# Kernel optimization log

Hardware: AMD Instinct MI355X
Metric: run time of the kernel (lower is better)

## Reference

```python
import jax, jax.numpy as jnp
import numpy as np

B, H, S, D = 4, 16, 2048, 64
INV_SCALE_FACTOR = 8.0  # scores are divided by this (== sqrt(D))
DROPOUT_P = 0.0         # deterministic baseline; dropout is identity at p=0


def setup_inputs() -> dict:
    key = jax.random.key(0)
    kq, kk, kv = jax.random.split(key, 3)
    return {
        "query": jax.random.normal(kq, (B, H, S, D), dtype=jnp.float32),
        "key": jax.random.normal(kk, (B, H, S, D), dtype=jnp.float32),
        "value": jax.random.normal(kv, (B, H, S, D), dtype=jnp.float32),
    }


def reference(query, key, value):
    # scores: [B, H, Sq, Sk]
    scores = jnp.einsum("bhqd,bhkd->bhqk", query, key) / INV_SCALE_FACTOR
    probs = jax.nn.softmax(scores, axis=-1)
    # dropout_p == 0.0 -> identity
    out = jnp.einsum("bhqk,bhkd->bhqd", probs, value)
    return out
```

## Files before the change

### kernel.cpp

```cpp
#include <hip/hip_runtime.h>


#define S_LEN 2048
#define D_DIM 64
#define TK    64
#define NTILE (S_LEN / TK)
#define LOG2E_OVER8 0.18033688011112042f
#define VROW  72
#define VTILE (64 * VROW)
#define VBH   (NTILE * VTILE)

typedef __bf16 bf16x8 __attribute__((ext_vector_type(8)));
typedef __bf16 bf16x4 __attribute__((ext_vector_type(4)));
typedef short  s16x4  __attribute__((ext_vector_type(4)));
typedef float  f32x4  __attribute__((ext_vector_type(4)));
typedef unsigned short us;

__device__ __forceinline__ us f2bf(float f) {
    union { __bf16 h; us u; } c;
    c.h = (__bf16)f;
    return c.u;
}

__device__ __forceinline__ unsigned pk2(float a, float b) {
#if __has_builtin(__builtin_amdgcn_cvt_pk_bf16_f32)
    typedef __bf16 bf2 __attribute__((ext_vector_type(2)));
    union { bf2 h; unsigned u; } c;
    c.h = __builtin_amdgcn_cvt_pk_bf16_f32(a, b);
    return c.u;
#else
    return ((unsigned)f2bf(b) << 16) | f2bf(a);
#endif
}

__device__ __forceinline__ float fast_exp2(float x) {
#if __has_builtin(__builtin_amdgcn_exp2f)
    return __builtin_amdgcn_exp2f(x);
#else
    return exp2f(x);
#endif
}

__device__ __forceinline__ void gload_lds16(const void* g, void* l) {
    __builtin_amdgcn_global_load_lds(
        (const __attribute__((address_space(1))) unsigned int*)g,
        (__attribute__((address_space(3))) unsigned int*)l, 16, 0, 0);
}

__device__ __forceinline__ f32x4 mfma16x16x16(s16x4 a, s16x4 b, f32x4 c) {
#if __has_builtin(__builtin_amdgcn_mfma_f32_16x16x16bf16_1k)
    return __builtin_amdgcn_mfma_f32_16x16x16bf16_1k(a, b, c, 0, 0, 0);
#else
    f32x4 d = c;
    asm volatile("v_mfma_f32_16x16x16_bf16 %0, %1, %2, %0"
                 : "+v"(d) : "v"(a), "v"(b));
    return d;
#endif
}

__global__ __launch_bounds__(256)
void prep(const float* __restrict__ K, const float* __restrict__ V,
          us* __restrict__ Kb, us* __restrict__ Vt) {
    __shared__ us Ls[64 * 68];
    const int bx = blockIdx.x, tid = threadIdx.x;
    if (bx < 4096) {
        const size_t i = ((size_t)bx * 256 + tid) * 8;
        const float4 a = *(const float4*)(K + i);
        const float4 b = *(const float4*)(K + i + 4);
        union { us u[8]; uint4 q; } pk;
        pk.u[0] = f2bf(a.x); pk.u[1] = f2bf(a.y);
        pk.u[2] = f2bf(a.z); pk.u[3] = f2bf(a.w);
        pk.u[4] = f2bf(b.x); pk.u[5] = f2bf(b.y);
        pk.u[6] = f2bf(b.z); pk.u[7] = f2bf(b.w);
        *(uint4*)(Kb + i) = pk.q;
    } else {
        const int idx = bx - 4096;
        const int t = idx & (NTILE - 1), bh = idx >> 5;
        {
            const int r = tid >> 2, seg = tid & 3;
            const float* src = V + ((size_t)bh * S_LEN + t * TK + r) * D_DIM + seg * 16;
            us* dst = &Ls[r * 68 + seg * 16];
#pragma unroll
            for (int i = 0; i < 2; ++i) {
                const float4 v0 = *(const float4*)(src + 8 * i);
                const float4 v1 = *(const float4*)(src + 8 * i + 4);
                union { us u[8]; uint2 q[2]; } pk;
                pk.u[0] = f2bf(v0.x); pk.u[1] = f2bf(v0.y);
                pk.u[2] = f2bf(v0.z); pk.u[3] = f2bf(v0.w);
                pk.u[4] = f2bf(v1.x); pk.u[5] = f2bf(v1.y);
                pk.u[6] = f2bf(v1.z); pk.u[7] = f2bf(v1.w);
                *(uint2*)(dst + 8 * i) = pk.q[0];
                *(uint2*)(dst + 8 * i + 4) = pk.q[1];
            }
        }
        __syncthreads();
        {
            const int d = tid >> 2, sc = tid & 3;
            union { us u[16]; uint4 q[2]; } pk;
#pragma unroll
            for (int j = 0; j < 16; ++j) pk.u[j] = Ls[(sc * 16 + j) * 68 + d];
            us* dst = Vt + (size_t)bh * VBH + t * VTILE + d * VROW + sc * 16;
            *(uint4*)(dst) = pk.q[0];
            *(uint4*)(dst + 8) = pk.q[1];
        }
    }
}

__global__ __launch_bounds__(256, 4)
void fa_fwd(const float* __restrict__ Qg, const us* __restrict__ Kb,
            const us* __restrict__ Vtb, float* __restrict__ Og) {
    __shared__ __align__(16) us Kl[2][TK * 64];
    __shared__ __align__(16) us Vl[2][VTILE];

    const int tid  = threadIdx.x;
    const int w    = tid >> 6;
    const int lane = tid & 63;
    const int l15  = lane & 15;
    const int quad = lane >> 4;
    const int x    = l15 & 7;

    const int bid   = blockIdx.x;
    const int chunk = bid >> 3;
    const int bh    = ((bid & 7) << 3) | (chunk >> 5);
    const int qb    = chunk & 31;
    const size_t base = (size_t)bh * S_LEN * D_DIM;

    bf16x8 bq0, bq1;
    {
        const float* qrow = Qg + base + (size_t)(qb * 64 + w * 16 + l15) * D_DIM + quad * 8;
        const float4 x0 = *(const float4*)qrow;
        const float4 x1 = *(const float4*)(qrow + 4);
        const float4 y0 = *(const float4*)(qrow + 32);
        const float4 y1 = *(const float4*)(qrow + 36);
        bq0[0]=(__bf16)(x0.x*LOG2E_OVER8); bq0[1]=(__bf16)(x0.y*LOG2E_OVER8);
        bq0[2]=(__bf16)(x0.z*LOG2E_OVER8); bq0[3]=(__bf16)(x0.w*LOG2E_OVER8);
        bq0[4]=(__bf16)(x1.x*LOG2E_OVER8); bq0[5]=(__bf16)(x1.y*LOG2E_OVER8);
        bq0[6]=(__bf16)(x1.z*LOG2E_OVER8); bq0[7]=(__bf16)(x1.w*LOG2E_OVER8);
        bq1[0]=(__bf16)(y0.x*LOG2E_OVER8); bq1[1]=(__bf16)(y0.y*LOG2E_OVER8);
        bq1[2]=(__bf16)(y0.z*LOG2E_OVER8); bq1[3]=(__bf16)(y0.w*LOG2E_OVER8);
        bq1[4]=(__bf16)(y1.x*LOG2E_OVER8); bq1[5]=(__bf16)(y1.y*LOG2E_OVER8);
        bq1[6]=(__bf16)(y1.z*LOG2E_OVER8); bq1[7]=(__bf16)(y1.w*LOG2E_OVER8);
    }

    const int krow   = w * 16 + (lane >> 3);
    const int kchunk = (lane & 7) ^ (lane >> 3);
    const us* ksrc = Kb + base + (size_t)krow * D_DIM + kchunk * 8;
    const us* vsrc = Vtb + (size_t)bh * VBH + lane * 8;

    f32x4 lv = {0.f, 0.f, 0.f, 0.f};
    f32x4 oa[4];
#pragma unroll
    for (int db = 0; db < 4; ++db) oa[db] = (f32x4){0.f, 0.f, 0.f, 0.f};

#pragma unroll
    for (int j = 0; j < 2; ++j)
        gload_lds16(ksrc + j * 512, &Kl[0][w * 1024 + j * 512]);
#pragma unroll
    for (int j = 0; j < 2; ++j)
        gload_lds16(vsrc + (w * 2 + j) * 512, &Vl[0][(w * 2 + j) * 512]);
    if (w == 0) gload_lds16(vsrc + 8 * 512, &Vl[0][8 * 512]);
    __syncthreads();

#pragma unroll 1
    for (int t = 0; t < NTILE; ++t) {
        const int cur = t & 1;
        if (t + 1 < NTILE) {
            const us* ks = ksrc + (size_t)(t + 1) * (TK * D_DIM);
            const us* vs = vsrc + (size_t)(t + 1) * VTILE;
            us* kd = &Kl[cur ^ 1][w * 1024];
            us* vd = &Vl[cur ^ 1][0];
#pragma unroll
            for (int j = 0; j < 2; ++j)
                gload_lds16(ks + j * 512, kd + j * 512);
#pragma unroll
            for (int j = 0; j < 2; ++j)
                gload_lds16(vs + (w * 2 + j) * 512, vd + (w * 2 + j) * 512);
            if (w == 0) gload_lds16(vs + 8 * 512, vd + 8 * 512);
        }

        const us* kl = Kl[cur];
        const us* vl = Vl[cur];
#pragma unroll
        for (int kb = 0; kb < 4; ++kb) {
            const int row = kb * 16 + l15;
            const bf16x8 a0 = *(const bf16x8*)&kl[row * 64 + ((quad ^ x) * 8)];
            const bf16x8 a1 = *(const bf16x8*)&kl[row * 64 + (((4 + quad) ^ x) * 8)];
            f32x4 c = {0.f, 0.f, 0.f, 0.f};
            c = __builtin_amdgcn_mfma_f32_16x16x32_bf16(a0, bq0, c, 0, 0, 0);
            c = __builtin_amdgcn_mfma_f32_16x16x32_bf16(a1, bq1, c, 0, 0, 0);

            const float p0 = fast_exp2(c[0]);
            const float p1 = fast_exp2(c[1]);
            const float p2 = fast_exp2(c[2]);
            const float p3 = fast_exp2(c[3]);
            lv += (f32x4){p0, p1, p2, p3};
            union { unsigned u[2]; s16x4 s; } bu;
            bu.u[0] = pk2(p0, p1);
            bu.u[1] = pk2(p2, p3);

#pragma unroll
            for (int db = 0; db < 4; ++db) {
                union { bf16x4 h; s16x4 s; } au;
                au.h = *(const bf16x4*)&vl[l15 * VROW + quad * 4 + db * (16 * VROW) + kb * 16];
                oa[db] = mfma16x16x16(au.s, bu.s, oa[db]);
            }
        }
        __syncthreads();
    }

    float l_q = lv[0] + lv[1] + lv[2] + lv[3];
    l_q += __shfl_xor(l_q, 16, 64);
    l_q += __shfl_xor(l_q, 32, 64);
    const float inv = 1.f / l_q;
    float* op = Og + base + (size_t)(qb * 64 + w * 16 + l15) * D_DIM + quad * 4;
#pragma unroll
    for (int db = 0; db < 4; ++db) {
        float4 v = { oa[db][0] * inv, oa[db][1] * inv, oa[db][2] * inv, oa[db][3] * inv };
        *(float4*)(op + db * 16) = v;
    }
}

extern "C" void kernel_launch(void* const* d_in, const int* in_sizes, int n_in,
                              void* d_out, int out_size, void* d_ws, size_t ws_size,
                              hipStream_t stream) {
    const float* Q = (const float*)d_in[0];
    const float* K = (const float*)d_in[1];
    const float* V = (const float*)d_in[2];
    float* O = (float*)d_out;

    us* Kb = (us*)d_ws;
    us* Vt = Kb + (size_t)64 * S_LEN * D_DIM;

    prep<<<4096 + 2048, 256, 0, stream>>>(K, V, Kb, Vt);
    fa_fwd<<<dim3(2048), 256, 0, stream>>>(Q, Kb, Vt, O);
}
```

Before: 230.0 us.

## Process two query sub-tiles per wave to reuse K/V tiles from LDS

Each workgroup now handles 128 query rows instead of 64, with each wave computing two 16-row query tiles that share the same K and V fragments read from LDS. This halves the number of workgroups and halves the global K/V traffic and LDS reads per query row. In exchange, register pressure roughly doubles for the accumulators, and fewer blocks (1024) may reduce occupancy and load balance across CUs.

```diff
diff --git a/kernel.cpp b/kernel.cpp
--- a/kernel.cpp
+++ b/kernel.cpp
@@ -121,25 +121,32 @@
 
     const int bid   = blockIdx.x;
     const int chunk = bid >> 3;
-    const int bh    = ((bid & 7) << 3) | (chunk >> 5);
-    const int qb    = chunk & 31;
+    const int bh    = ((bid & 7) << 3) | (chunk >> 4);
+    const int qb    = chunk & 15;
     const size_t base = (size_t)bh * S_LEN * D_DIM;
 
-    bf16x8 bq0, bq1;
+    bf16x8 bq00, bq01, bq10, bq11;
     {
-        const float* qrow = Qg + base + (size_t)(qb * 64 + w * 16 + l15) * D_DIM + quad * 8;
-        const float4 x0 = *(const float4*)qrow;
-        const float4 x1 = *(const float4*)(qrow + 4);
-        const float4 y0 = *(const float4*)(qrow + 32);
-        const float4 y1 = *(const float4*)(qrow + 36);
-        bq0[0]=(__bf16)(x0.x*LOG2E_OVER8); bq0[1]=(__bf16)(x0.y*LOG2E_OVER8);
-        bq0[2]=(__bf16)(x0.z*LOG2E_OVER8); bq0[3]=(__bf16)(x0.w*LOG2E_OVER8);
-        bq0[4]=(__bf16)(x1.x*LOG2E_OVER8); bq0[5]=(__bf16)(x1.y*LOG2E_OVER8);
-        bq0[6]=(__bf16)(x1.z*LOG2E_OVER8); bq0[7]=(__bf16)(x1.w*LOG2E_OVER8);
-        bq1[0]=(__bf16)(y0.x*LOG2E_OVER8); bq1[1]=(__bf16)(y0.y*LOG2E_OVER8);
-        bq1[2]=(__bf16)(y0.z*LOG2E_OVER8); bq1[3]=(__bf16)(y0.w*LOG2E_OVER8);
-        bq1[4]=(__bf16)(y1.x*LOG2E_OVER8); bq1[5]=(__bf16)(y1.y*LOG2E_OVER8);
-        bq1[6]=(__bf16)(y1.z*LOG2E_OVER8); bq1[7]=(__bf16)(y1.w*LOG2E_OVER8);
+        const float* q0 = Qg + base + (size_t)(qb * 128 + w * 32 + l15) * D_DIM + quad * 8;
+        const float* q1 = q0 + 16 * D_DIM;
+#define LOADQ(dst0, dst1, p)                                                  \
+        {                                                                     \
+            const float4 x0 = *(const float4*)(p);                            \
+            const float4 x1 = *(const float4*)((p) + 4);                      \
+            const float4 y0 = *(const float4*)((p) + 32);                     \
+            const float4 y1 = *(const float4*)((p) + 36);                     \
+            dst0[0]=(__bf16)(x0.x*LOG2E_OVER8); dst0[1]=(__bf16)(x0.y*LOG2E_OVER8); \
+            dst0[2]=(__bf16)(x0.z*LOG2E_OVER8); dst0[3]=(__bf16)(x0.w*LOG2E_OVER8); \
+            dst0[4]=(__bf16)(x1.x*LOG2E_OVER8); dst0[5]=(__bf16)(x1.y*LOG2E_OVER8); \
+            dst0[6]=(__bf16)(x1.z*LOG2E_OVER8); dst0[7]=(__bf16)(x1.w*LOG2E_OVER8); \
+            dst1[0]=(__bf16)(y0.x*LOG2E_OVER8); dst1[1]=(__bf16)(y0.y*LOG2E_OVER8); \
+            dst1[2]=(__bf16)(y0.z*LOG2E_OVER8); dst1[3]=(__bf16)(y0.w*LOG2E_OVER8); \
+            dst1[4]=(__bf16)(y1.x*LOG2E_OVER8); dst1[5]=(__bf16)(y1.y*LOG2E_OVER8); \
+            dst1[6]=(__bf16)(y1.z*LOG2E_OVER8); dst1[7]=(__bf16)(y1.w*LOG2E_OVER8); \
+        }
+        LOADQ(bq00, bq01, q0)
+        LOADQ(bq10, bq11, q1)
+#undef LOADQ
     }
 
     const int krow   = w * 16 + (lane >> 3);
@@ -147,10 +154,13 @@
     const us* ksrc = Kb + base + (size_t)krow * D_DIM + kchunk * 8;
     const us* vsrc = Vtb + (size_t)bh * VBH + lane * 8;
 
-    f32x4 lv = {0.f, 0.f, 0.f, 0.f};
-    f32x4 oa[4];
-#pragma unroll
-    for (int db = 0; db < 4; ++db) oa[db] = (f32x4){0.f, 0.f, 0.f, 0.f};
+    f32x4 lv0 = {0.f, 0.f, 0.f, 0.f}, lv1 = {0.f, 0.f, 0.f, 0.f};
+    f32x4 oa0[4], oa1[4];
+#pragma unroll
+    for (int db = 0; db < 4; ++db) {
+        oa0[db] = (f32x4){0.f, 0.f, 0.f, 0.f};
+        oa1[db] = (f32x4){0.f, 0.f, 0.f, 0.f};
+    }
 
 #pragma unroll
     for (int j = 0; j < 2; ++j)
@@ -185,38 +195,58 @@
             const int row = kb * 16 + l15;
             const bf16x8 a0 = *(const bf16x8*)&kl[row * 64 + ((quad ^ x) * 8)];
             const bf16x8 a1 = *(const bf16x8*)&kl[row * 64 + (((4 + quad) ^ x) * 8)];
-            f32x4 c = {0.f, 0.f, 0.f, 0.f};
-            c = __builtin_amdgcn_mfma_f32_16x16x32_bf16(a0, bq0, c, 0, 0, 0);
-            c = __builtin_amdgcn_mfma_f32_16x16x32_bf16(a1, bq1, c, 0, 0, 0);
-
-            const float p0 = fast_exp2(c[0]);
-            const float p1 = fast_exp2(c[1]);
-            const float p2 = fast_exp2(c[2]);
-            const float p3 = fast_exp2(c[3]);
-            lv += (f32x4){p0, p1, p2, p3};
-            union { unsigned u[2]; s16x4 s; } bu;
-            bu.u[0] = pk2(p0, p1);
-            bu.u[1] = pk2(p2, p3);
+            f32x4 c0 = {0.f, 0.f, 0.f, 0.f};
+            c0 = __builtin_amdgcn_mfma_f32_16x16x32_bf16(a0, bq00, c0, 0, 0, 0);
+            c0 = __builtin_amdgcn_mfma_f32_16x16x32_bf16(a1, bq01, c0, 0, 0, 0);
+            f32x4 c1 = {0.f, 0.f, 0.f, 0.f};
+            c1 = __builtin_amdgcn_mfma_f32_16x16x32_bf16(a0, bq10, c1, 0, 0, 0);
+            c1 = __builtin_amdgcn_mfma_f32_16x16x32_bf16(a1, bq11, c1, 0, 0, 0);
+
+            const float p00 = fast_exp2(c0[0]);
+            const float p01 = fast_exp2(c0[1]);
+            const float p02 = fast_exp2(c0[2]);
+            const float p03 = fast_exp2(c0[3]);
+            lv0 += (f32x4){p00, p01, p02, p03};
+            const float p10 = fast_exp2(c1[0]);
+            const float p11 = fast_exp2(c1[1]);
+            const float p12 = fast_exp2(c1[2]);
+            const float p13 = fast_exp2(c1[3]);
+            lv1 += (f32x4){p10, p11, p12, p13};
+            union { unsigned u[2]; s16x4 s; } bu0, bu1;
+            bu0.u[0] = pk2(p00, p01);
+            bu0.u[1] = pk2(p02, p03);
+            bu1.u[0] = pk2(p10, p11);
+            bu1.u[1] = pk2(p12, p13);
 
 #pragma unroll
             for (int db = 0; db < 4; ++db) {
                 union { bf16x4 h; s16x4 s; } au;
                 au.h = *(const bf16x4*)&vl[l15 * VROW + quad * 4 + db * (16 * VROW) + kb * 16];
-                oa[db] = mfma16x16x16(au.s, bu.s, oa[db]);
+                oa0[db] = mfma16x16x16(au.s, bu0.s, oa0[db]);
+                oa1[db] = mfma16x16x16(au.s, bu1.s, oa1[db]);
             }
         }
         __syncthreads();
     }
 
-    float l_q = lv[0] + lv[1] + lv[2] + lv[3];
-    l_q += __shfl_xor(l_q, 16, 64);
-    l_q += __shfl_xor(l_q, 32, 64);
-    const float inv = 1.f / l_q;
-    float* op = Og + base + (size_t)(qb * 64 + w * 16 + l15) * D_DIM + quad * 4;
+    float lq0 = lv0[0] + lv0[1] + lv0[2] + lv0[3];
+    lq0 += __shfl_xor(lq0, 16, 64);
+    lq0 += __shfl_xor(lq0, 32, 64);
+    float lq1 = lv1[0] + lv1[1] + lv1[2] + lv1[3];
+    lq1 += __shfl_xor(lq1, 16, 64);
+    lq1 += __shfl_xor(lq1, 32, 64);
+    const float inv0 = 1.f / lq0;
+    const float inv1 = 1.f / lq1;
+    float* op0 = Og + base + (size_t)(qb * 128 + w * 32 + l15) * D_DIM + quad * 4;
+    float* op1 = op0 + 16 * D_DIM;
 #pragma unroll
     for (int db = 0; db < 4; ++db) {
-        float4 v = { oa[db][0] * inv, oa[db][1] * inv, oa[db][2] * inv, oa[db][3] * inv };
-        *(float4*)(op + db * 16) = v;
+        float4 v0 = { oa0[db][0] * inv0, oa0[db][1] * inv0,
+                      oa0[db][2] * inv0, oa0[db][3] * inv0 };
+        *(float4*)(op0 + db * 16) = v0;
+        float4 v1 = { oa1[db][0] * inv1, oa1[db][1] * inv1,
+                      oa1[db][2] * inv1, oa1[db][3] * inv1 };
+        *(float4*)(op1 + db * 16) = v1;
     }
 }
 
@@ -232,5 +262,5 @@
     us* Vt = Kb + (size_t)64 * S_LEN * D_DIM;
 
     prep<<<4096 + 2048, 256, 0, stream>>>(K, V, Kb, Vt);
-    fa_fwd<<<dim3(2048), 256, 0, stream>>>(Q, Kb, Vt, O);
-}
+    fa_fwd<<<dim3(1024), 256, 0, stream>>>(Q, Kb, Vt, O);
+}
```

Result: slower. 235.1 us (+2.2%).
